# Performance work log

Measured on AMD Instinct MI355X. Metric: run time of the kernel, lower is better.

The kernel has to match this reference:

```python
import jax, jax.numpy as jnp
import numpy as np

B, N, C, D = 16, 2048, 256, 256


def setup_inputs() -> dict:
    key = jax.random.key(0)
    ks = jax.random.split(key, 8)
    x = jax.random.normal(ks[0], (B, N, C), dtype=jnp.float32)
    valid_len = jax.random.randint(ks[1], (B,), 0, N)
    # nn.Linear params: weight [out, in], bias [out]
    s = 1.0 / np.sqrt(C)
    Wq = jax.random.uniform(ks[2], (D, C), dtype=jnp.float32, minval=-s, maxval=s)
    bq = jax.random.uniform(ks[3], (D,), dtype=jnp.float32, minval=-s, maxval=s)
    Wk = jax.random.uniform(ks[4], (D, C), dtype=jnp.float32, minval=-s, maxval=s)
    bk = jax.random.uniform(ks[5], (D,), dtype=jnp.float32, minval=-s, maxval=s)
    Wv = jax.random.uniform(ks[6], (D, C), dtype=jnp.float32, minval=-s, maxval=s)
    bv = jax.random.uniform(ks[7], (D,), dtype=jnp.float32, minval=-s, maxval=s)
    return {"x": x, "valid_len": valid_len, "Wq": Wq, "bq": bq,
            "Wk": Wk, "bk": bk, "Wv": Wv, "bv": bv}


def reference(x, valid_len, Wq, bq, Wk, bk, Wv, bv):
    # QKV projections (nn.Linear: x @ W^T + b)
    q = jnp.einsum('bnc,dc->bnd', x, Wq) + bq
    k = jnp.einsum('bnc,dc->bnd', x, Wk) + bk
    v = jnp.einsum('bnc,dc->bnd', x, Wv) + bv
    # scores [B, N, N] = q @ k^T (no scaling: scale_factor_d unused in forward)
    scores = jnp.einsum('bnd,bmd->bnm', q, k)
    # key-side valid-length mask: arange(N) < valid_len[b], broadcast over queries
    mask = jnp.arange(N)[None, :] < valid_len[:, None]          # [B, N]
    scores = jnp.where(mask[:, None, :], scores, jnp.float32(-1000000.0))
    attn = jax.nn.softmax(scores, axis=-1)
    return jnp.einsum('bnm,bmd->bnd', attn, v)
```

## Files before the change

### kernel.cpp

```cpp
#include <hip/hip_runtime.h>
#include <hip/hip_bf16.h>
#include <stdint.h>

typedef __attribute__((ext_vector_type(8))) _Float16 half8;
typedef __attribute__((ext_vector_type(4))) _Float16 half4;
typedef __attribute__((ext_vector_type(2))) __fp16 fp16x2;
typedef __attribute__((ext_vector_type(4))) float f32x4;
typedef __attribute__((ext_vector_type(16))) float f32x16;
typedef __attribute__((ext_vector_type(4))) float float4v;

#define DEVI static __device__ __forceinline__

constexpr int Bb = 16, Nn = 2048, Cc = 256, Dd = 256;

DEVI unsigned short f2h_bits(float f) {
  _Float16 h = (_Float16)f;
  union { _Float16 h; unsigned short u; } c;
  c.h = h;
  return c.u;
}

DEVI void gl_lds16(const void* gsrc, void* ldst) {
  __builtin_amdgcn_global_load_lds(
      (const __attribute__((address_space(1))) unsigned int*)gsrc,
      (__attribute__((address_space(3))) unsigned int*)ldst, 16, 0, 0);
}

DEVI f32x4 mfma16h(half8 a, half8 b, f32x4 c) {
  return __builtin_amdgcn_mfma_f32_16x16x32_f16(a, b, c, 0, 0, 0);
}
DEVI f32x16 mfma32h(half8 a, half8 b, f32x16 c) {
  return __builtin_amdgcn_mfma_f32_32x32x16_f16(a, b, c, 0, 0, 0);
}

DEVI unsigned int pkrtz(float a, float b) {
  union { fp16x2 h; unsigned int u; } c;
  c.h = __builtin_amdgcn_cvt_pkrtz(a, b);
  return c.u;
}

__global__ void k_split(const float* __restrict__ x, const float* __restrict__ wq,
                        const float* __restrict__ wk, const float* __restrict__ wv,
                        _Float16* __restrict__ xh, _Float16* __restrict__ wh) {
  int i = blockIdx.x * 256 + threadIdx.x;
  if (i < 2097152) {
    float4v v = reinterpret_cast<const float4v*>(x)[i];
    half4 h;
#pragma unroll
    for (int j = 0; j < 4; ++j) h[j] = (_Float16)v[j];
    reinterpret_cast<half4*>(xh)[i] = h;
  } else {
    int ii = i - 2097152;
    int mat = ii >> 16;
    int rem = ii & 65535;
    const float* w = (mat == 0) ? wq : ((mat == 1) ? wk : wv);
    wh[(size_t)mat * 65536 + rem] = (_Float16)w[rem];
  }
}

__global__ __launch_bounds__(256, 2) void k_qkv(
    const _Float16* __restrict__ xh, const _Float16* __restrict__ wh,
    const float* __restrict__ bq, const float* __restrict__ bk, const float* __restrict__ bv,
    _Float16* __restrict__ qout, _Float16* __restrict__ kout, _Float16* __restrict__ vt) {
  __shared__ __align__(16) unsigned short smem[17408];

  const int tid = threadIdx.x;
  const int m0 = blockIdx.x * 128;
  const int n0 = blockIdx.y * 128;
  const int mat = blockIdx.z;
  const _Float16* wmat = wh + (size_t)mat * 65536;
  const int wave = tid >> 6, lane = tid & 63;
  const int wr = wave >> 1, wc = wave & 1;
  const int l15 = lane & 15, lq = lane >> 4;

  f32x4 zero4 = {0.f, 0.f, 0.f, 0.f};
  f32x4 acc[4][4];
#pragma unroll
  for (int a = 0; a < 4; ++a)
#pragma unroll
    for (int b2 = 0; b2 < 4; ++b2) acc[a][b2] = zero4;

  char* As = (char*)smem;
  char* Bs = (char*)smem + 16384;

  for (int kc = 0; kc < 4; ++kc) {
#pragma unroll
    for (int i = 0; i < 4; ++i) {
      int p = i * 4096 + tid * 16;
      int row = p >> 7;
      int src_in_row = (p & 127) ^ ((row & 7) << 4);
      const char* g = (const char*)(xh + (size_t)(m0 + row) * Cc + kc * 64) + src_in_row;
      gl_lds16(g, As + p);
    }
#pragma unroll
    for (int i = 0; i < 4; ++i) {
      int p = i * 4096 + tid * 16;
      int row = p >> 7;
      int src_in_row = (p & 127) ^ ((row & 7) << 4);
      const char* g = (const char*)(wmat + (size_t)(n0 + row) * Cc + kc * 64) + src_in_row;
      gl_lds16(g, Bs + p);
    }
    __syncthreads();
#pragma unroll
    for (int ks = 0; ks < 2; ++ks) {
      half8 af[4], bfr[4];
#pragma unroll
      for (int mf = 0; mf < 4; ++mf) {
        int row = wr * 64 + mf * 16 + l15;
        int byte = (row * 128 + ks * 64 + lq * 16) ^ ((row & 7) << 4);
        af[mf] = *(const half8*)(As + byte);
      }
#pragma unroll
      for (int nf = 0; nf < 4; ++nf) {
        int row = wc * 64 + nf * 16 + l15;
        int byte = (row * 128 + ks * 64 + lq * 16) ^ ((row & 7) << 4);
        bfr[nf] = *(const half8*)(Bs + byte);
      }
#pragma unroll
      for (int mf = 0; mf < 4; ++mf)
#pragma unroll
        for (int nf = 0; nf < 4; ++nf) acc[mf][nf] = mfma16h(af[mf], bfr[nf], acc[mf][nf]);
    }
    __syncthreads();
  }

  const float* bias = (mat == 0) ? bq : ((mat == 1) ? bk : bv);
  if (mat < 2) {
    _Float16* oo = (mat == 0) ? qout : kout;
#pragma unroll
    for (int nf = 0; nf < 4; ++nf) {
      int col = n0 + wc * 64 + nf * 16 + l15;
      float bval = bias[col];
#pragma unroll
      for (int mf = 0; mf < 4; ++mf) {
        int grow = m0 + wr * 64 + mf * 16 + lq * 4;
#pragma unroll
        for (int r = 0; r < 4; ++r)
          oo[(size_t)(grow + r) * Dd + col] = (_Float16)(acc[mf][nf][r] + bval);
      }
    }
  } else {
    __syncthreads();
#pragma unroll
    for (int nf = 0; nf < 4; ++nf) {
      int dl = wc * 64 + nf * 16 + l15;
      float bval = bias[n0 + dl];
#pragma unroll
      for (int mf = 0; mf < 4; ++mf) {
        int nl = wr * 64 + mf * 16 + lq * 4;
#pragma unroll
        for (int r = 0; r < 4; ++r) smem[dl * 136 + nl + r] = f2h_bits(acc[mf][nf][r] + bval);
      }
    }
    __syncthreads();
    const int bbat = m0 >> 11, tok0 = m0 & 2047;
#pragma unroll
    for (int pss = 0; pss < 8; ++pss) {
      int idx = pss * 256 + tid;
      int dl = idx >> 4;
      int cu = idx & 15;
      half8 vval = *(const half8*)((const char*)smem + dl * 272 + cu * 16);
      size_t off = ((size_t)bbat * Dd + n0 + dl) * Nn + tok0 + cu * 8;
      *(half8*)(vt + off) = vval;
    }
  }
}

__global__ __launch_bounds__(512, 2) void k_attn(
    const _Float16* __restrict__ qg, const _Float16* __restrict__ kin,
    const _Float16* __restrict__ vt, const int* __restrict__ vlen,
    float* __restrict__ out) {
  __shared__ __align__(16) char SMEM[149504];
  char* const KVb = SMEM;
  unsigned int* const PL = (unsigned int*)(SMEM + 131072);
  float* const mex = (float*)(SMEM + 147456);
  float* const lex = (float*)(SMEM + 148480);

  const int tid = threadIdx.x;
  const int wave = tid >> 6, lane = tid & 63;
  const int l31 = lane & 31, h = lane >> 5;
  const int wq = wave >> 1, wk = wave & 1;
  const int id = blockIdx.x;
  const int g = id & 7;
  const int j = id >> 3;
  const int b = g + 8 * (j >> 4);
  const int q0 = (j & 15) * 128;
  const int L = vlen[b];
  const bool uni = (L == 0);
  const int Lk = uni ? Nn : L;
  const int nt = (Lk + 63) >> 6;

  const char* kbase = (const char*)(kin + (size_t)b * Nn * Dd);
  const char* vbase = (const char*)(vt + (size_t)b * Dd * Nn);
  const char* qbase = (const char*)(qg + ((size_t)b * Nn + q0) * Dd);

  auto STAGE = [&](int buf, int t) {
    char* dst = KVb + buf * 65536;
    const int k0 = t * 64;
#pragma unroll
    for (int i = 0; i < 4; ++i) {
      int p = i * 8192 + tid * 16;
      int row = p >> 9;
      int sl = ((p & 511) >> 4) ^ (row & 31);
      gl_lds16(kbase + (size_t)(k0 + row) * 512 + (sl << 4), dst + p);
    }
#pragma unroll
    for (int i = 0; i < 4; ++i) {
      int p = i * 8192 + tid * 16;
      int r = p >> 9;
      int sl = ((p & 511) >> 4) ^ (r & 31);
      int cl = sl << 4;
      int d = r * 4 + (cl >> 7);
      int kbyte = cl & 127;
      gl_lds16(vbase + (size_t)d * (Nn * 2) + (size_t)k0 * 2 + kbyte, dst + 32768 + p);
    }
  };

  STAGE(0, 0);
#pragma unroll
  for (int i = 0; i < 8; ++i) {
    int p = i * 8192 + tid * 16;
    int row = p >> 9;
    int sl = ((p & 511) >> 4) ^ (row & 31);
    gl_lds16(qbase + (size_t)row * 512 + (sl << 4), KVb + 65536 + p);
  }
  asm volatile("s_waitcnt vmcnt(0)" ::: "memory");
  asm volatile("s_barrier" ::: "memory");

  half8 qreg[16];
  {
    const int row = wq * 32 + l31;
#pragma unroll
    for (int kt = 0; kt < 16; ++kt) {
      int byte = row * 512 + (((kt * 2 + h) ^ (row & 31)) << 4);
      qreg[kt] = *(const half8*)(KVb + 65536 + byte);
    }
  }
  asm volatile("s_waitcnt lgkmcnt(0)" ::: "memory");
  asm volatile("s_barrier" ::: "memory");

  f32x16 acc[4];
#pragma unroll
  for (int dg = 0; dg < 4; ++dg)
#pragma unroll
    for (int r = 0; r < 16; ++r) acc[dg][r] = 0.f;
  float m = -__builtin_inff();
  float lsum = 0.f;

  for (int t = 0; t < nt; ++t) {
    const int cur = t & 1;
    if (t + 1 < nt) {
      STAGE(cur ^ 1, t + 1);
      asm volatile("s_waitcnt vmcnt(8)" ::: "memory");
    } else {
      asm volatile("s_waitcnt vmcnt(0)" ::: "memory");
    }
    asm volatile("s_barrier" ::: "memory");

    const char* Ks = KVb + cur * 65536;
    const char* Vs = Ks + 32768;
    const int k0 = t * 64;

    f32x16 st;
#pragma unroll
    for (int r = 0; r < 16; ++r) st[r] = 0.f;
    if (!uni) {
      const int key = wk * 32 + l31;
      __builtin_amdgcn_s_setprio(1);
#pragma unroll
      for (int kt = 0; kt < 16; ++kt) {
        int byte = key * 512 + (((kt * 2 + h) ^ l31) << 4);
        half8 kf = *(const half8*)(Ks + byte);
        st = mfma32h(kf, qreg[kt], st);
      }
      __builtin_amdgcn_s_setprio(0);
      if (k0 + 64 > L) {
#pragma unroll
        for (int r = 0; r < 16; ++r) {
          int keyg = k0 + wk * 32 + (r & 3) + 8 * (r >> 2) + 4 * h;
          if (keyg >= L) st[r] = -1e6f;
        }
      }
    }

    float pm = st[0];
#pragma unroll
    for (int r = 1; r < 16; ++r) pm = fmaxf(pm, st[r]);
    pm = fmaxf(pm, __shfl_xor(pm, 32));
    if (lane < 32) mex[wave * 32 + lane] = pm;
    asm volatile("s_waitcnt lgkmcnt(0)\ns_barrier" ::: "memory");
    float pmo = mex[(wave ^ 1) * 32 + l31];
    float mnew = fmaxf(m, fmaxf(pm, pmo));
    float scale = __expf(m - mnew);
    m = mnew;
    float psum = 0.f;
#pragma unroll
    for (int r = 0; r < 16; ++r) {
      float p_ = __expf(st[r] - mnew);
      st[r] = p_;
      psum += p_;
    }
    lsum = lsum * scale + psum;

#pragma unroll
    for (int i = 0; i < 8; ++i) {
      unsigned int pk = pkrtz(st[2 * i], st[2 * i + 1]);
      int kp = wk * 16 + 4 * (i >> 1) + (i & 1) + 2 * h;
      PL[wq * 1024 + kp * 32 + l31] = pk;
    }

    if (!__all(scale == 1.0f)) {
#pragma unroll
      for (int dg = 0; dg < 4; ++dg)
#pragma unroll
        for (int r = 0; r < 16; ++r) acc[dg][r] *= scale;
    }

    asm volatile("s_waitcnt lgkmcnt(0)\ns_barrier" ::: "memory");

    union { unsigned int u[4]; half8 v; } pf0, pf1, pf2, pf3;
#pragma unroll
    for (int w = 0; w < 4; ++w) {
      pf0.u[w] = PL[wq * 1024 + (0 * 8 + h * 4 + w) * 32 + l31];
      pf1.u[w] = PL[wq * 1024 + (1 * 8 + h * 4 + w) * 32 + l31];
      pf2.u[w] = PL[wq * 1024 + (2 * 8 + h * 4 + w) * 32 + l31];
      pf3.u[w] = PL[wq * 1024 + (3 * 8 + h * 4 + w) * 32 + l31];
    }

    __builtin_amdgcn_s_setprio(1);
#pragma unroll
    for (int dg = 0; dg < 4; ++dg) {
      int r = wk * 32 + dg * 8 + (l31 >> 2);
#pragma unroll
      for (int ks = 0; ks < 4; ++ks) {
        int slot = (l31 & 3) * 8 + ks * 2 + h;
        half8 vf = *(const half8*)(Vs + r * 512 + ((slot ^ (r & 31)) << 4));
        acc[dg] = mfma32h(vf, ks == 0 ? pf0.v : (ks == 1 ? pf1.v : (ks == 2 ? pf2.v : pf3.v)),
                          acc[dg]);
      }
    }
    __builtin_amdgcn_s_setprio(0);

    asm volatile("s_barrier" ::: "memory");
  }

  lsum += __shfl_xor(lsum, 32);
  if (lane < 32) lex[wave * 32 + lane] = lsum;
  asm volatile("s_waitcnt lgkmcnt(0)\ns_barrier" ::: "memory");
  float linv = 1.f / (lsum + lex[(wave ^ 1) * 32 + l31]);

  float* T = (float*)SMEM;
  {
    const int ql = wq * 32 + l31;
#pragma unroll
    for (int dg = 0; dg < 4; ++dg)
#pragma unroll
      for (int r = 0; r < 16; ++r) {
        int d = wk * 128 + dg * 32 + (r & 3) + 8 * (r >> 2) + 4 * h;
        T[ql * 260 + d] = acc[dg][r] * linv;
      }
  }
  asm volatile("s_waitcnt lgkmcnt(0)\ns_barrier" ::: "memory");

  {
    const int rb = tid >> 6;
    const int c4 = (tid & 63) * 4;
#pragma unroll
    for (int i = 0; i < 16; ++i) {
      int row = rb + i * 8;
      float4v v = *(const float4v*)(T + row * 260 + c4);
      *(float4v*)(out + ((size_t)b * Nn + q0 + row) * Dd + c4) = v;
    }
  }
}

extern "C" void kernel_launch(void* const* d_in, const int* in_sizes, int n_in,
                              void* d_out, int out_size, void* d_ws, size_t ws_size,
                              hipStream_t stream) {
  const float* x = (const float*)d_in[0];
  const int* vlen = (const int*)d_in[1];
  const float* Wq = (const float*)d_in[2];
  const float* bq = (const float*)d_in[3];
  const float* Wk = (const float*)d_in[4];
  const float* bk = (const float*)d_in[5];
  const float* Wv = (const float*)d_in[6];
  const float* bv = (const float*)d_in[7];
  float* out = (float*)d_out;
  char* ws = (char*)d_ws;

  _Float16* qh = (_Float16*)(ws);
  _Float16* kk = (_Float16*)(ws + 16777216);
  _Float16* vt = (_Float16*)(ws + 33554432);
  _Float16* wh = (_Float16*)(ws + 50331648);
  _Float16* xh = (_Float16*)d_out;

  k_split<<<8960, 256, 0, stream>>>(x, Wq, Wk, Wv, xh, wh);
  k_qkv<<<dim3(256, 2, 3), 256, 0, stream>>>(xh, wh, bq, bk, bv, qh, kk, vt);
  k_attn<<<256, 512, 0, stream>>>(qh, kk, vt, vlen, out);
}
```

Before: 122.2 us.

## Split attention over key halves with partial outputs and combine kernel

Adds a split-K flash attention kernel that gives each block 64 queries and one half of the key range, writing fp16 partial outputs plus per-row max and sum to workspace. A separate combine kernel merges the two halves into the final output. This raises the block count from 256 to 1024, which should improve CU occupancy and load balance when valid lengths vary, at the cost of extra global traffic and a third launch. The old kernel's conditional rescale is also made unconditional and moved after the P loads. The new path is used only when the workspace is large enough.

After: 129.5 us. 6.0% more time.

```diff
diff --git a/kernel.cpp b/kernel.cpp
--- a/kernel.cpp
+++ b/kernel.cpp
@@ -164,6 +164,243 @@
       *(half8*)(vt + off) = vval;
     }
   }
+}
+
+__global__ __launch_bounds__(256, 2) void k_attn_p(
+    const _Float16* __restrict__ qg, const _Float16* __restrict__ kin,
+    const _Float16* __restrict__ vt, const int* __restrict__ vlen,
+    _Float16* __restrict__ Op, float* __restrict__ ml) {
+  __shared__ __align__(16) char SMEM[66048];
+  char* const Kb = SMEM;
+  char* const Vb = SMEM + 32768;
+  unsigned int* const PL = (unsigned int*)SMEM;
+  float* const mex = (float*)(SMEM + 65536);
+
+  const int tid = threadIdx.x;
+  const int wave = tid >> 6, lane = tid & 63;
+  const int l31 = lane & 31, h = lane >> 5;
+  const int wq = wave >> 1, wk = wave & 1;
+  const int id = blockIdx.x;
+  const int g = id & 7;
+  const int b = g + 8 * (id >> 9);
+  const int q0 = ((id >> 4) & 31) * 64;
+  const int kh = (id >> 3) & 1;
+  const int kst = kh * 1024;
+  const int L = vlen[b];
+  const bool uni = (L == 0);
+  const int Lk = uni ? Nn : L;
+  const int avail = Lk - kst;
+  const int nt = (avail > 0) ? ((avail + 63) >> 6 < 16 ? (avail + 63) >> 6 : 16) : 0;
+  const size_t prow = (size_t)(b * 2 + kh) * Nn + q0;
+
+  if (nt == 0) {
+    if (tid < 64) {
+      ml[(prow + tid) * 2 + 0] = -1e30f;
+      ml[(prow + tid) * 2 + 1] = 0.f;
+    }
+    return;
+  }
+
+  const char* kbase = (const char*)(kin + (size_t)b * Nn * Dd);
+  const char* vbase = (const char*)(vt + (size_t)b * Dd * Nn);
+  const char* qbase = (const char*)(qg + ((size_t)b * Nn + q0) * Dd);
+
+#pragma unroll
+  for (int i = 0; i < 8; ++i) {
+    int p = i * 4096 + tid * 16;
+    int row = p >> 9;
+    int sl = ((p & 511) >> 4) ^ (row & 31);
+    gl_lds16(qbase + (size_t)row * 512 + (sl << 4), Kb + p);
+  }
+  asm volatile("s_waitcnt vmcnt(0)" ::: "memory");
+  asm volatile("s_barrier" ::: "memory");
+  half8 qreg[16];
+  {
+    const int row = wq * 32 + l31;
+#pragma unroll
+    for (int kt = 0; kt < 16; ++kt) {
+      int byte = row * 512 + (((kt * 2 + h) ^ (row & 31)) << 4);
+      qreg[kt] = *(const half8*)(Kb + byte);
+    }
+  }
+  asm volatile("s_waitcnt lgkmcnt(0)" ::: "memory");
+  asm volatile("s_barrier" ::: "memory");
+
+  f32x16 acc[4];
+#pragma unroll
+  for (int dg = 0; dg < 4; ++dg)
+#pragma unroll
+    for (int r = 0; r < 16; ++r) acc[dg][r] = 0.f;
+  float m = -__builtin_inff();
+  float lsum = 0.f;
+
+  for (int t = 0; t < nt; ++t) {
+    const int k0 = kst + t * 64;
+#pragma unroll
+    for (int i = 0; i < 8; ++i) {
+      int p = i * 4096 + tid * 16;
+      int row = p >> 9;
+      int sl = ((p & 511) >> 4) ^ (row & 31);
+      gl_lds16(kbase + (size_t)(k0 + row) * 512 + (sl << 4), Kb + p);
+    }
+#pragma unroll
+    for (int i = 0; i < 8; ++i) {
+      int p = i * 4096 + tid * 16;
+      int r = p >> 9;
+      int sl = ((p & 511) >> 4) ^ (r & 31);
+      int cl = sl << 4;
+      int d = r * 4 + (cl >> 7);
+      int kbyte = cl & 127;
+      gl_lds16(vbase + (size_t)d * (Nn * 2) + (size_t)k0 * 2 + kbyte, Vb + p);
+    }
+    asm volatile("s_waitcnt vmcnt(0)" ::: "memory");
+    asm volatile("s_barrier" ::: "memory");
+
+    f32x16 st;
+#pragma unroll
+    for (int r = 0; r < 16; ++r) st[r] = 0.f;
+    if (!uni) {
+      const int key = wk * 32 + l31;
+      __builtin_amdgcn_s_setprio(1);
+#pragma unroll
+      for (int kt = 0; kt < 16; ++kt) {
+        int byte = key * 512 + (((kt * 2 + h) ^ l31) << 4);
+        half8 kf = *(const half8*)(Kb + byte);
+        st = mfma32h(kf, qreg[kt], st);
+      }
+      __builtin_amdgcn_s_setprio(0);
+      if (k0 + 64 > L) {
+#pragma unroll
+        for (int r = 0; r < 16; ++r) {
+          int keyg = k0 + wk * 32 + (r & 3) + 8 * (r >> 2) + 4 * h;
+          if (keyg >= L) st[r] = -1e6f;
+        }
+      }
+    }
+
+    float pm = st[0];
+#pragma unroll
+    for (int r = 1; r < 16; ++r) pm = fmaxf(pm, st[r]);
+    pm = fmaxf(pm, __shfl_xor(pm, 32));
+    if (lane < 32) mex[wave * 32 + lane] = pm;
+    asm volatile("s_waitcnt lgkmcnt(0)\ns_barrier" ::: "memory");
+    float pmo = mex[(wave ^ 1) * 32 + l31];
+    float mnew = fmaxf(m, fmaxf(pm, pmo));
+    float scale = __expf(m - mnew);
+    m = mnew;
+    float psum = 0.f;
+#pragma unroll
+    for (int r = 0; r < 16; ++r) {
+      float p_ = __expf(st[r] - mnew);
+      st[r] = p_;
+      psum += p_;
+    }
+    lsum = lsum * scale + psum;
+
+#pragma unroll
+    for (int i = 0; i < 8; ++i) {
+      unsigned int pk = pkrtz(st[2 * i], st[2 * i + 1]);
+      int kp = wk * 16 + 4 * (i >> 1) + (i & 1) + 2 * h;
+      PL[wq * 1024 + kp * 32 + l31] = pk;
+    }
+    asm volatile("s_waitcnt lgkmcnt(0)\ns_barrier" ::: "memory");
+
+    union { unsigned int u[4]; half8 v; } pf0, pf1, pf2, pf3;
+#pragma unroll
+    for (int w = 0; w < 4; ++w) {
+      pf0.u[w] = PL[wq * 1024 + (0 * 8 + h * 4 + w) * 32 + l31];
+      pf1.u[w] = PL[wq * 1024 + (1 * 8 + h * 4 + w) * 32 + l31];
+      pf2.u[w] = PL[wq * 1024 + (2 * 8 + h * 4 + w) * 32 + l31];
+      pf3.u[w] = PL[wq * 1024 + (3 * 8 + h * 4 + w) * 32 + l31];
+    }
+
+#pragma unroll
+    for (int dg = 0; dg < 4; ++dg)
+#pragma unroll
+      for (int r = 0; r < 16; ++r) acc[dg][r] *= scale;
+
+    __builtin_amdgcn_s_setprio(1);
+#pragma unroll
+    for (int dg = 0; dg < 4; ++dg) {
+      int r = wk * 32 + dg * 8 + (l31 >> 2);
+#pragma unroll
+      for (int ks = 0; ks < 4; ++ks) {
+        int slot = (l31 & 3) * 8 + ks * 2 + h;
+        half8 vf = *(const half8*)(Vb + r * 512 + ((slot ^ (r & 31)) << 4));
+        acc[dg] = mfma32h(vf, ks == 0 ? pf0.v : (ks == 1 ? pf1.v : (ks == 2 ? pf2.v : pf3.v)),
+                          acc[dg]);
+      }
+    }
+    __builtin_amdgcn_s_setprio(0);
+
+    asm volatile("s_barrier" ::: "memory");
+  }
+
+  lsum += __shfl_xor(lsum, 32);
+  if (lane < 32) mex[wave * 32 + lane] = lsum;
+  asm volatile("s_waitcnt lgkmcnt(0)\ns_barrier" ::: "memory");
+  float ltot = lsum + mex[(wave ^ 1) * 32 + l31];
+  float linv = 1.f / ltot;
+
+  if (h == 0 && wk == 0) {
+    size_t qq = prow + wq * 32 + l31;
+    ml[qq * 2 + 0] = m;
+    ml[qq * 2 + 1] = ltot;
+  }
+
+  _Float16* T = (_Float16*)SMEM;
+  {
+    const int ql = wq * 32 + l31;
+#pragma unroll
+    for (int dg = 0; dg < 4; ++dg)
+#pragma unroll
+      for (int r = 0; r < 16; ++r) {
+        int d = wk * 128 + dg * 32 + (r & 3) + 8 * (r >> 2) + 4 * h;
+        T[ql * 264 + d] = (_Float16)(acc[dg][r] * linv);
+      }
+  }
+  asm volatile("s_waitcnt lgkmcnt(0)\ns_barrier" ::: "memory");
+
+  {
+    const int rb = tid >> 6;
+    const int c4 = (tid & 63) * 4;
+#pragma unroll
+    for (int i = 0; i < 16; ++i) {
+      int row = rb + i * 4;
+      half4 v = *(const half4*)(T + row * 264 + c4);
+      *(half4*)(Op + (prow + row) * Dd + c4) = v;
+    }
+  }
+}
+
+__global__ __launch_bounds__(256) void k_comb(const _Float16* __restrict__ Op,
+                                              const float* __restrict__ ml,
+                                              float* __restrict__ out) {
+  int rid = blockIdx.x * 4 + (threadIdx.x >> 6);
+  int lane = threadIdx.x & 63;
+  int b = rid >> 11, q = rid & 2047;
+  size_t i0 = (size_t)(b * 2 + 0) * Nn + q;
+  size_t i1 = (size_t)(b * 2 + 1) * Nn + q;
+  float m0 = ml[i0 * 2], l0 = ml[i0 * 2 + 1];
+  float m1 = ml[i1 * 2], l1 = ml[i1 * 2 + 1];
+  float M = fmaxf(m0, m1);
+  float c0 = (l0 > 0.f) ? __expf(m0 - M) * l0 : 0.f;
+  float c1 = (l1 > 0.f) ? __expf(m1 - M) * l1 : 0.f;
+  float inv = 1.f / (c0 + c1);
+  c0 *= inv;
+  c1 *= inv;
+  float4v o = {0.f, 0.f, 0.f, 0.f};
+  {
+    half4 o0 = *(const half4*)(Op + i0 * 256 + lane * 4);
+#pragma unroll
+    for (int j = 0; j < 4; ++j) o[j] = c0 * (float)o0[j];
+  }
+  if (c1 > 0.f) {
+    half4 o1 = *(const half4*)(Op + i1 * 256 + lane * 4);
+#pragma unroll
+    for (int j = 0; j < 4; ++j) o[j] += c1 * (float)o1[j];
+  }
+  *(float4v*)(out + ((size_t)b * Nn + q) * 256 + lane * 4) = o;
 }
 
 __global__ __launch_bounds__(512, 2) void k_attn(
@@ -308,14 +545,6 @@
       int kp = wk * 16 + 4 * (i >> 1) + (i & 1) + 2 * h;
       PL[wq * 1024 + kp * 32 + l31] = pk;
     }
-
-    if (!__all(scale == 1.0f)) {
-#pragma unroll
-      for (int dg = 0; dg < 4; ++dg)
-#pragma unroll
-        for (int r = 0; r < 16; ++r) acc[dg][r] *= scale;
-    }
-
     asm volatile("s_waitcnt lgkmcnt(0)\ns_barrier" ::: "memory");
 
     union { unsigned int u[4]; half8 v; } pf0, pf1, pf2, pf3;
@@ -326,6 +555,11 @@
       pf2.u[w] = PL[wq * 1024 + (2 * 8 + h * 4 + w) * 32 + l31];
       pf3.u[w] = PL[wq * 1024 + (3 * 8 + h * 4 + w) * 32 + l31];
     }
+
+#pragma unroll
+    for (int dg = 0; dg < 4; ++dg)
+#pragma unroll
+      for (int r = 0; r < 16; ++r) acc[dg][r] *= scale;
 
     __builtin_amdgcn_s_setprio(1);
 #pragma unroll
@@ -392,9 +626,16 @@
   _Float16* kk = (_Float16*)(ws + 16777216);
   _Float16* vt = (_Float16*)(ws + 33554432);
   _Float16* wh = (_Float16*)(ws + 50331648);
+  _Float16* Op = (_Float16*)(ws + 51380224);
+  float* ml = (float*)(ws + 84934656);
   _Float16* xh = (_Float16*)d_out;
 
   k_split<<<8960, 256, 0, stream>>>(x, Wq, Wk, Wv, xh, wh);
   k_qkv<<<dim3(256, 2, 3), 256, 0, stream>>>(xh, wh, bq, bk, bv, qh, kk, vt);
-  k_attn<<<256, 512, 0, stream>>>(qh, kk, vt, vlen, out);
-}
+  if (ws_size >= 85458944ull) {
+    k_attn_p<<<1024, 256, 0, stream>>>(qh, kk, vt, vlen, Op, ml);
+    k_comb<<<8192, 256, 0, stream>>>(Op, ml, out);
+  } else {
+    k_attn<<<256, 512, 0, stream>>>(qh, kk, vt, vlen, out);
+  }
+}
```
